# Kernel tuning notes

Measured on AMD Instinct MI355X. Metric: run time of the kernel, lower is better.

Reference implementation:

```python
import jax, jax.numpy as jnp
import numpy as np

N_NODES = 100000
N_EDGES = 640000
D_IN = 128
D_H = 128


def _lin_params(key, fan_in, fan_out):
    kw, kb = jax.random.split(key)
    s = 1.0 / np.sqrt(fan_in)
    W = jax.random.uniform(kw, (fan_in, fan_out), jnp.float32, -s, s)
    b = jax.random.uniform(kb, (fan_out,), jnp.float32, -s, s)
    return W, b


def setup_inputs() -> dict:
    key = jax.random.key(0)
    ks = jax.random.split(key, 9)
    x = jax.random.normal(ks[0], (N_NODES, D_IN), jnp.float32)
    edge_index = jax.random.randint(ks[1], (2, N_EDGES), 0, N_NODES, dtype=jnp.int64)
    W1, b1 = _lin_params(ks[2], D_IN, D_H)
    W2, b2 = _lin_params(ks[3], D_H, D_H)
    W3, b3 = _lin_params(ks[4], D_H, D_H)
    Wg0, bg0 = _lin_params(ks[5], D_H, D_H)
    Wg1, bg1 = _lin_params(ks[6], D_H, D_H)
    Wo, bo = _lin_params(ks[7], D_H, 1)
    return {"x": x, "edge_index": edge_index,
            "W1": W1, "b1": b1, "W2": W2, "b2": b2, "W3": W3, "b3": b3,
            "Wg0": Wg0, "bg0": bg0, "Wg1": Wg1, "bg1": bg1, "Wo": Wo, "bo": bo}


def gcn_conv(x, src, dst, W, b, n_nodes):
    """PyG GCNConv: D^{-1/2} (A+I) D^{-1/2} X W + b (self-loops added, sym norm)."""
    h = x @ W  # [N, F_out]
    # degree of A+I counted on target side (each self-loop adds 1)
    deg = jnp.zeros((n_nodes,), x.dtype).at[dst].add(1.0) + 1.0
    dis = jax.lax.rsqrt(deg)  # deg^{-1/2}
    coef = dis[src] * dis[dst]  # [E]
    agg = jax.ops.segment_sum(h[src] * coef[:, None], dst, num_segments=n_nodes)
    out = agg + h * (dis * dis)[:, None]  # self-loop term
    return out + b


def reference(x, edge_index, W1, b1, W2, b2, W3, b3, Wg0, bg0, Wg1, bg1, Wo, bo):
    src, dst = edge_index[0], edge_index[1]
    n = x.shape[0]
    lrelu = jax.nn.leaky_relu  # slope 0.01, matches torch default
    # feature extractor MLP
    h = lrelu(x @ W1 + b1)
    h = lrelu(h @ W2 + b2)
    h = lrelu(h @ W3 + b3)
    # input GCN
    h = lrelu(gcn_conv(h, src, dst, Wg0, bg0, n))
    # hidden GCN (dropout is identity in eval mode)
    h = lrelu(gcn_conv(h, src, dst, Wg1, bg1, n))
    # output GCN -> scalar per node
    return gcn_conv(h, src, dst, Wo, bo, n)
```

## Files before the change

kernel.cpp:

```cpp
#include <hip/hip_runtime.h>
#include <hip/hip_bf16.h>

#define D_H 128

typedef __attribute__((ext_vector_type(8))) short bf16x8;
typedef __attribute__((ext_vector_type(4))) float f32x4;

__device__ inline void trunc_split(float x, ushort& hi, ushort& lo) {
    uint u = __builtin_bit_cast(uint, x);
    hi = (ushort)(u >> 16);
    float fh = __builtin_bit_cast(float, u & 0xFFFF0000u);
    float fl = x - fh;
    lo = (ushort)(__builtin_bit_cast(uint, fl) >> 16);
}


__global__ __launch_bounds__(256)
void deg_count_int_kernel(const int* __restrict__ dst, int* __restrict__ cnt, int E) {
    int e = blockIdx.x * 256 + threadIdx.x;
    if (e < E) atomicAdd(&cnt[dst[e]], 1);
}

__global__ __launch_bounds__(256)
void dis_finalize_kernel(const int* __restrict__ cnt, float* __restrict__ dis, int M) {
    int i = blockIdx.x * 256 + threadIdx.x;
    if (i < M) dis[i] = rsqrtf((float)cnt[i] + 1.0f);
}

__global__ __launch_bounds__(256)
void scan_blocks_kernel(const int* __restrict__ cnt, int* __restrict__ rowptr,
                        int* __restrict__ aux, int M) {
    __shared__ int sdata[256];
    const int base = blockIdx.x * 1024 + threadIdx.x * 4;
    int v[4];
#pragma unroll
    for (int i = 0; i < 4; ++i) v[i] = (base + i < M) ? cnt[base + i] : 0;
    int tsum = v[0] + v[1] + v[2] + v[3];
    sdata[threadIdx.x] = tsum;
    __syncthreads();
    int val = tsum;
    for (int off = 1; off < 256; off <<= 1) {
        int n = (threadIdx.x >= off) ? sdata[threadIdx.x - off] : 0;
        __syncthreads();
        val += n;
        sdata[threadIdx.x] = val;
        __syncthreads();
    }
    int run = val - tsum;
#pragma unroll
    for (int i = 0; i < 4; ++i) {
        if (base + i < M) rowptr[base + i] = run;
        run += v[i];
    }
    if (threadIdx.x == 255) aux[blockIdx.x] = val;
}

__global__ __launch_bounds__(128)
void scan_aux_kernel(int* __restrict__ aux, int n) {
    __shared__ int s[128];
    int v = (threadIdx.x < n) ? aux[threadIdx.x] : 0;
    s[threadIdx.x] = v;
    __syncthreads();
    int val = v;
    for (int off = 1; off < 128; off <<= 1) {
        int nn = (threadIdx.x >= off) ? s[threadIdx.x - off] : 0;
        __syncthreads();
        val += nn;
        s[threadIdx.x] = val;
        __syncthreads();
    }
    if (threadIdx.x < n) aux[threadIdx.x] = val - v;
}

__global__ __launch_bounds__(256)
void scan_add_kernel(int* __restrict__ rowptr, int* __restrict__ cursor,
                     const int* __restrict__ aux, int M) {
    int i = blockIdx.x * 256 + threadIdx.x;
    if (i >= M) return;
    int v = rowptr[i] + aux[i >> 10];
    rowptr[i] = v;
    cursor[i] = v;
}

__global__ __launch_bounds__(256)
void scatter_kernel(const int* __restrict__ src, const int* __restrict__ dst,
                    const float* __restrict__ dis, int* __restrict__ cursor,
                    int* __restrict__ es, float* __restrict__ ces, int E) {
    int e = blockIdx.x * 256 + threadIdx.x;
    if (e >= E) return;
    int s = src[e], d = dst[e];
    int pos = atomicAdd(&cursor[d], 1);
    es[pos] = s;
    ces[pos] = dis[s];
}

__global__ __launch_bounds__(256)
void wprep_kernel(const float* __restrict__ W1, const float* __restrict__ W2,
                  const float* __restrict__ W3, const float* __restrict__ W4,
                  const float* __restrict__ W5, ushort* __restrict__ imgs) {
    int w = blockIdx.x >> 6;
    int e = (blockIdx.x & 63) * 256 + threadIdx.x;
    const float* W = w == 0 ? W1 : w == 1 ? W2 : w == 2 ? W3 : w == 3 ? W4 : W5;
    int k = e >> 7, n = e & 127;
    ushort hi, lo;
    trunc_split(W[e], hi, lo);
    ushort* img = imgs + (size_t)w * 34816;
    img[n * 136 + k]         = hi;
    img[17408 + n * 136 + k] = lo;
}

__global__ __launch_bounds__(512, 2)
void fused_mlp4_kernel(const float* __restrict__ X, const ushort* __restrict__ imgs,
                       const float* __restrict__ b1, const float* __restrict__ b2,
                       const float* __restrict__ b3, float* __restrict__ Y, int M) {
    __shared__ ushort sW[34816];
    __shared__ ushort sXhi[17408];
    __shared__ ushort sXlo[17408];

    const int tid  = threadIdx.x;
    const int lane = tid & 63;
    const int wv   = tid >> 6;
    const int bn   = lane & 15;
    const int g    = lane >> 4;
    const int kof  = g * 8;
    const int row0 = blockIdx.x * 128;
    const int lrow = wv * 16 + bn;
    const int arow = row0 + lrow;

    bf16x8 ahi[4], alo[4];
    {
        const bool ok = arow < M;
        const float* ap = X + (size_t)arow * 128 + kof;
#pragma unroll
        for (int kb = 0; kb < 4; ++kb) {
            float f[8];
            if (ok) {
                float4 f0 = *(const float4*)(ap + kb * 32);
                float4 f1 = *(const float4*)(ap + kb * 32 + 4);
                f[0] = f0.x; f[1] = f0.y; f[2] = f0.z; f[3] = f0.w;
                f[4] = f1.x; f[5] = f1.y; f[6] = f1.z; f[7] = f1.w;
            } else {
#pragma unroll
                for (int e = 0; e < 8; ++e) f[e] = 0.f;
            }
            bf16x8 h, l;
#pragma unroll
            for (int e = 0; e < 8; ++e) {
                ushort hb, lb;
                trunc_split(f[e], hb, lb);
                h[e] = (short)hb; l[e] = (short)lb;
            }
            ahi[kb] = h; alo[kb] = l;
        }
    }

    f32x4 acc[8];
    for (int t = 0; t < 4; ++t) {
        if (t > 0) __syncthreads();
        {
            const uint4* g4 = (const uint4*)(imgs + (size_t)t * 34816);
            uint4*       s4 = (uint4*)sW;
#pragma unroll
            for (int j = 0; j < 9; ++j) {
                int c = j * 512 + tid;
                if (c < 4352) s4[c] = g4[c];
            }
        }
        if (t > 0) {
#pragma unroll
            for (int kb = 0; kb < 4; ++kb) {
                ahi[kb] = *(const bf16x8*)&sXhi[lrow * 136 + kb * 32 + kof];
                alo[kb] = *(const bf16x8*)&sXlo[lrow * 136 + kb * 32 + kof];
            }
        }
        __syncthreads();

#pragma unroll
        for (int nt = 0; nt < 8; ++nt) acc[nt] = (f32x4){0.f, 0.f, 0.f, 0.f};
#pragma unroll
        for (int kb = 0; kb < 4; ++kb) {
#pragma unroll
            for (int nt = 0; nt < 8; ++nt) {
                const ushort* ph = &sW[(nt * 16 + bn) * 136 + kb * 32 + kof];
                bf16x8 bh = *(const bf16x8*)ph;
                bf16x8 bl = *(const bf16x8*)(ph + 17408);
                acc[nt] = __builtin_amdgcn_mfma_f32_16x16x32_bf16(ahi[kb], bh, acc[nt], 0, 0, 0);
                acc[nt] = __builtin_amdgcn_mfma_f32_16x16x32_bf16(alo[kb], bh, acc[nt], 0, 0, 0);
                acc[nt] = __builtin_amdgcn_mfma_f32_16x16x32_bf16(ahi[kb], bl, acc[nt], 0, 0, 0);
            }
        }

        if (t < 3) {
            const float* bias = t == 0 ? b1 : t == 1 ? b2 : b3;
#pragma unroll
            for (int nt = 0; nt < 8; ++nt) {
                int col = nt * 16 + bn;
                float bc = bias[col];
#pragma unroll
                for (int i = 0; i < 4; ++i) {
                    float v = acc[nt][i] + bc;
                    v = v > 0.f ? v : 0.01f * v;
                    ushort h, l;
                    trunc_split(v, h, l);
                    int r = wv * 16 + g * 4 + i;
                    sXhi[r * 136 + col] = h;
                    sXlo[r * 136 + col] = l;
                }
            }
        } else {
#pragma unroll
            for (int nt = 0; nt < 8; ++nt) {
                int col = nt * 16 + bn;
#pragma unroll
                for (int i = 0; i < 4; ++i) {
                    int row = row0 + wv * 16 + g * 4 + i;
                    if (row < M) Y[(size_t)row * 128 + col] = acc[nt][i];
                }
            }
        }
    }
}

__global__ __launch_bounds__(512, 4)
void gemm128_mfma_kernel(const float* __restrict__ X, const ushort* __restrict__ img,
                         float* __restrict__ Y, int M) {
    __shared__ ushort sB[34816];

    const int tid  = threadIdx.x;
    const int lane = tid & 63;
    const int wv   = tid >> 6;
    const int bn   = lane & 15;
    const int g    = lane >> 4;
    const int kof  = g * 8;
    const int row0 = blockIdx.x * 128;
    const int arow = row0 + wv * 16 + bn;

    {
        const uint4* g4 = (const uint4*)img;
        uint4*       s4 = (uint4*)sB;
#pragma unroll
        for (int j = 0; j < 9; ++j) {
            int c = j * 512 + tid;
            if (c < 4352) s4[c] = g4[c];
        }
    }

    bf16x8 ahi[4], alo[4];
    {
        const bool ok = arow < M;
        const float* ap = X + (size_t)arow * 128 + kof;
#pragma unroll
        for (int kb = 0; kb < 4; ++kb) {
            float f[8];
            if (ok) {
                float4 f0 = *(const float4*)(ap + kb * 32);
                float4 f1 = *(const float4*)(ap + kb * 32 + 4);
                f[0] = f0.x; f[1] = f0.y; f[2] = f0.z; f[3] = f0.w;
                f[4] = f1.x; f[5] = f1.y; f[6] = f1.z; f[7] = f1.w;
            } else {
#pragma unroll
                for (int e = 0; e < 8; ++e) f[e] = 0.f;
            }
            bf16x8 h, l;
#pragma unroll
            for (int e = 0; e < 8; ++e) {
                ushort hb, lb;
                trunc_split(f[e], hb, lb);
                h[e] = (short)hb; l[e] = (short)lb;
            }
            ahi[kb] = h; alo[kb] = l;
        }
    }
    __syncthreads();

    f32x4 acc[8];
#pragma unroll
    for (int nt = 0; nt < 8; ++nt) acc[nt] = (f32x4){0.f, 0.f, 0.f, 0.f};
#pragma unroll
    for (int kb = 0; kb < 4; ++kb) {
#pragma unroll
        for (int nt = 0; nt < 8; ++nt) {
            const ushort* ph = &sB[(nt * 16 + bn) * 136 + kb * 32 + kof];
            bf16x8 bh = *(const bf16x8*)ph;
            bf16x8 bl = *(const bf16x8*)(ph + 17408);
            acc[nt] = __builtin_amdgcn_mfma_f32_16x16x32_bf16(ahi[kb], bh, acc[nt], 0, 0, 0);
            acc[nt] = __builtin_amdgcn_mfma_f32_16x16x32_bf16(alo[kb], bh, acc[nt], 0, 0, 0);
            acc[nt] = __builtin_amdgcn_mfma_f32_16x16x32_bf16(ahi[kb], bl, acc[nt], 0, 0, 0);
        }
    }

#pragma unroll
    for (int nt = 0; nt < 8; ++nt) {
        int col = nt * 16 + bn;
#pragma unroll
        for (int i = 0; i < 4; ++i) {
            int row = row0 + wv * 16 + g * 4 + i;
            if (row < M) Y[(size_t)row * 128 + col] = acc[nt][i];
        }
    }
}

template<int MODE>
__global__ __launch_bounds__(256)
void gcn_agg_csr_kernel(const float* __restrict__ H, const int* __restrict__ es,
                        const float* __restrict__ ces, const int* __restrict__ rowptr,
                        const int* __restrict__ cnt, const float* __restrict__ dis,
                        const float* __restrict__ bias, const float* __restrict__ Wo,
                        float* __restrict__ Y, float* __restrict__ ho, int M) {
    int w    = (blockIdx.x * 256 + threadIdx.x) >> 6;
    int lane = threadIdx.x & 63;
    if (w >= M) return;

    const float dd  = dis[w];
    const int   beg = rowptr[w];
    const int   n   = cnt[w];

    float2 hv = ((const float2*)H)[(size_t)w * 64 + lane];
    float2 acc;
    acc.x = hv.x * dd * dd;
    acc.y = hv.y * dd * dd;

    int j = 0;
    for (; j + 4 <= n; j += 4) {
        int   s0 = es[beg + j],      s1 = es[beg + j + 1];
        int   s2 = es[beg + j + 2],  s3 = es[beg + j + 3];
        float c0 = ces[beg + j] * dd,     c1 = ces[beg + j + 1] * dd;
        float c2 = ces[beg + j + 2] * dd, c3 = ces[beg + j + 3] * dd;
        float2 v0 = ((const float2*)H)[(size_t)s0 * 64 + lane];
        float2 v1 = ((const float2*)H)[(size_t)s1 * 64 + lane];
        float2 v2 = ((const float2*)H)[(size_t)s2 * 64 + lane];
        float2 v3 = ((const float2*)H)[(size_t)s3 * 64 + lane];
        acc.x += c0 * v0.x + c1 * v1.x + c2 * v2.x + c3 * v3.x;
        acc.y += c0 * v0.y + c1 * v1.y + c2 * v2.y + c3 * v3.y;
    }
    for (; j < n; ++j) {
        int   s = es[beg + j];
        float c = ces[beg + j] * dd;
        float2 v = ((const float2*)H)[(size_t)s * 64 + lane];
        acc.x += c * v.x;
        acc.y += c * v.y;
    }

    float2 bb = ((const float2*)bias)[lane];
    acc.x += bb.x; acc.y += bb.y;
    acc.x = acc.x > 0.f ? acc.x : 0.01f * acc.x;
    acc.y = acc.y > 0.f ? acc.y : 0.01f * acc.y;

    if (MODE == 1) {
        ((float2*)Y)[(size_t)w * 64 + lane] = acc;
    } else {
        float2 wv = ((const float2*)Wo)[lane];
        float p = acc.x * wv.x + acc.y * wv.y;
#pragma unroll
        for (int off = 32; off > 0; off >>= 1) p += __shfl_down(p, off, 64);
        if (lane == 0) ho[w] = p;
    }
}

__global__ __launch_bounds__(256)
void out_csr_kernel(const float* __restrict__ ho, const int* __restrict__ es,
                    const float* __restrict__ ces, const int* __restrict__ rowptr,
                    const int* __restrict__ cnt, const float* __restrict__ dis,
                    const float* __restrict__ bo, float* __restrict__ out, int M) {
    int i = blockIdx.x * 256 + threadIdx.x;
    if (i >= M) return;
    float dd  = dis[i];
    float acc = ho[i] * dd * dd;
    int   beg = rowptr[i], n = cnt[i];
    for (int j = 0; j < n; ++j)
        acc += ces[beg + j] * dd * ho[es[beg + j]];
    out[i] = acc + bo[0];
}


extern "C" void kernel_launch(void* const* d_in, const int* in_sizes, int n_in,
                              void* d_out, int out_size, void* d_ws, size_t ws_size,
                              hipStream_t stream) {
    const float* x   = (const float*)d_in[0];
    const int*   ei  = (const int*)d_in[1];
    const float* W1  = (const float*)d_in[2];
    const float* b1  = (const float*)d_in[3];
    const float* W2  = (const float*)d_in[4];
    const float* b2  = (const float*)d_in[5];
    const float* W3  = (const float*)d_in[6];
    const float* b3  = (const float*)d_in[7];
    const float* Wg0 = (const float*)d_in[8];
    const float* bg0 = (const float*)d_in[9];
    const float* Wg1 = (const float*)d_in[10];
    const float* bg1 = (const float*)d_in[11];
    const float* Wo  = (const float*)d_in[12];
    const float* bo  = (const float*)d_in[13];

    const int M = in_sizes[0] / D_H;
    const int E = in_sizes[1] / 2;
    const int* se = ei;
    const int* de = ei + E;

    float*  A      = (float*)d_ws;
    float*  B      = A + (size_t)M * D_H;
    ushort* Wimg   = (ushort*)(B + (size_t)M * D_H);
    float*  dis    = (float*)(Wimg + 5 * 34816);
    float*  ho     = dis + M;
    float*  ces    = ho + M;
    int*    cnt    = (int*)(ces + E);
    int*    rowptr = cnt + M;
    int*    cursor = rowptr + M;
    int*    es     = cursor + M;
    int*    aux    = es + E;

    float* out = (float*)d_out;

    const int nChunks     = (M + 1023) / 1024;
    const int gemm_blocks = (M + 127) / 128;
    const int node_waves  = (M * 64 + 255) / 256;

    hipMemsetAsync(cnt, 0, M * sizeof(int), stream);
    wprep_kernel<<<320, 256, 0, stream>>>(W1, W2, W3, Wg0, Wg1, Wimg);
    deg_count_int_kernel<<<(E + 255) / 256, 256, 0, stream>>>(de, cnt, E);
    scan_blocks_kernel<<<nChunks, 256, 0, stream>>>(cnt, rowptr, aux, M);
    scan_aux_kernel<<<1, 128, 0, stream>>>(aux, nChunks);
    scan_add_kernel<<<(M + 255) / 256, 256, 0, stream>>>(rowptr, cursor, aux, M);
    dis_finalize_kernel<<<(M + 255) / 256, 256, 0, stream>>>(cnt, dis, M);
    scatter_kernel<<<(E + 255) / 256, 256, 0, stream>>>(se, de, dis, cursor, es, ces, E);

    fused_mlp4_kernel<<<gemm_blocks, 512, 0, stream>>>(x, Wimg, b1, b2, b3, B, M);

    gcn_agg_csr_kernel<1><<<node_waves, 256, 0, stream>>>(B, es, ces, rowptr, cnt, dis, bg0, nullptr, A, nullptr, M);

    gemm128_mfma_kernel<<<gemm_blocks, 512, 0, stream>>>(A, Wimg + 4 * 34816, B, M);

    gcn_agg_csr_kernel<2><<<node_waves, 256, 0, stream>>>(B, es, ces, rowptr, cnt, dis, bg1, Wo, nullptr, ho, M);

    out_csr_kernel<<<(M + 255) / 256, 256, 0, stream>>>(ho, es, ces, rowptr, cnt, dis, bo, out, M);
}
```

Before: 317.7 us.

## Cut fused MLP shared memory by aliasing activations and widen GEMM per-wave tiles

The fused MLP kernel drops its separate hi/lo activation buffers. It stages fp32 activations in the weight buffer, reloads them into registers and splits them to bf16 hi/lo there, with extra barriers. This cuts LDS use from about 139 KB to 70 KB so more blocks can fit per CU. The standalone GEMM now uses 256 threads, with each wave computing two 16-row groups that reuse every B fragment loaded from LDS. This halves LDS traffic per MFMA but raises register pressure.

```diff
diff --git a/kernel.cpp b/kernel.cpp
--- a/kernel.cpp
+++ b/kernel.cpp
@@ -109,13 +109,12 @@
     img[17408 + n * 136 + k] = lo;
 }
 
-__global__ __launch_bounds__(512, 2)
+__global__ __launch_bounds__(512, 4)
 void fused_mlp4_kernel(const float* __restrict__ X, const ushort* __restrict__ imgs,
                        const float* __restrict__ b1, const float* __restrict__ b2,
                        const float* __restrict__ b3, float* __restrict__ Y, int M) {
     __shared__ ushort sW[34816];
-    __shared__ ushort sXhi[17408];
-    __shared__ ushort sXlo[17408];
+    float* sAct = (float*)sW;
 
     const int tid  = threadIdx.x;
     const int lane = tid & 63;
@@ -125,10 +124,10 @@
     const int kof  = g * 8;
     const int row0 = blockIdx.x * 128;
     const int lrow = wv * 16 + bn;
-    const int arow = row0 + lrow;
 
     bf16x8 ahi[4], alo[4];
     {
+        const int arow = row0 + lrow;
         const bool ok = arow < M;
         const float* ap = X + (size_t)arow * 128 + kof;
 #pragma unroll
@@ -156,7 +155,6 @@
 
     f32x4 acc[8];
     for (int t = 0; t < 4; ++t) {
-        if (t > 0) __syncthreads();
         {
             const uint4* g4 = (const uint4*)(imgs + (size_t)t * 34816);
             uint4*       s4 = (uint4*)sW;
@@ -164,13 +162,6 @@
             for (int j = 0; j < 9; ++j) {
                 int c = j * 512 + tid;
                 if (c < 4352) s4[c] = g4[c];
-            }
-        }
-        if (t > 0) {
-#pragma unroll
-            for (int kb = 0; kb < 4; ++kb) {
-                ahi[kb] = *(const bf16x8*)&sXhi[lrow * 136 + kb * 32 + kof];
-                alo[kb] = *(const bf16x8*)&sXlo[lrow * 136 + kb * 32 + kof];
             }
         }
         __syncthreads();
@@ -191,6 +182,7 @@
         }
 
         if (t < 3) {
+            __syncthreads();
             const float* bias = t == 0 ? b1 : t == 1 ? b2 : b3;
 #pragma unroll
             for (int nt = 0; nt < 8; ++nt) {
@@ -200,13 +192,25 @@
                 for (int i = 0; i < 4; ++i) {
                     float v = acc[nt][i] + bc;
                     v = v > 0.f ? v : 0.01f * v;
-                    ushort h, l;
-                    trunc_split(v, h, l);
-                    int r = wv * 16 + g * 4 + i;
-                    sXhi[r * 136 + col] = h;
-                    sXlo[r * 136 + col] = l;
+                    sAct[(wv * 16 + g * 4 + i) * 132 + col] = v;
                 }
             }
+            __syncthreads();
+#pragma unroll
+            for (int kb = 0; kb < 4; ++kb) {
+                float4 f0 = *(const float4*)&sAct[lrow * 132 + kb * 32 + kof];
+                float4 f1 = *(const float4*)&sAct[lrow * 132 + kb * 32 + kof + 4];
+                float f[8] = {f0.x, f0.y, f0.z, f0.w, f1.x, f1.y, f1.z, f1.w};
+                bf16x8 h, l;
+#pragma unroll
+                for (int e = 0; e < 8; ++e) {
+                    ushort hb, lb;
+                    trunc_split(f[e], hb, lb);
+                    h[e] = (short)hb; l[e] = (short)lb;
+                }
+                ahi[kb] = h; alo[kb] = l;
+            }
+            __syncthreads();
         } else {
 #pragma unroll
             for (int nt = 0; nt < 8; ++nt) {
@@ -221,7 +225,7 @@
     }
 }
 
-__global__ __launch_bounds__(512, 4)
+__global__ __launch_bounds__(256, 2)
 void gemm128_mfma_kernel(const float* __restrict__ X, const ushort* __restrict__ img,
                          float* __restrict__ Y, int M) {
     __shared__ ushort sB[34816];
@@ -232,21 +236,19 @@
     const int bn   = lane & 15;
     const int g    = lane >> 4;
     const int kof  = g * 8;
-    const int row0 = blockIdx.x * 128;
-    const int arow = row0 + wv * 16 + bn;
+    const int row0 = blockIdx.x * 128 + wv * 32;
 
     {
         const uint4* g4 = (const uint4*)img;
         uint4*       s4 = (uint4*)sB;
 #pragma unroll
-        for (int j = 0; j < 9; ++j) {
-            int c = j * 512 + tid;
-            if (c < 4352) s4[c] = g4[c];
-        }
-    }
-
-    bf16x8 ahi[4], alo[4];
-    {
+        for (int j = 0; j < 17; ++j) s4[j * 256 + tid] = g4[j * 256 + tid];
+    }
+
+    bf16x8 ahi[2][4], alo[2][4];
+#pragma unroll
+    for (int rg = 0; rg < 2; ++rg) {
+        const int arow = row0 + rg * 16 + bn;
         const bool ok = arow < M;
         const float* ap = X + (size_t)arow * 128 + kof;
 #pragma unroll
@@ -268,14 +270,18 @@
                 trunc_split(f[e], hb, lb);
                 h[e] = (short)hb; l[e] = (short)lb;
             }
-            ahi[kb] = h; alo[kb] = l;
+            ahi[rg][kb] = h; alo[rg][kb] = l;
         }
     }
     __syncthreads();
 
-    f32x4 acc[8];
-#pragma unroll
-    for (int nt = 0; nt < 8; ++nt) acc[nt] = (f32x4){0.f, 0.f, 0.f, 0.f};
+    f32x4 acc0[8], acc1[8];
+#pragma unroll
+    for (int nt = 0; nt < 8; ++nt) {
+        acc0[nt] = (f32x4){0.f, 0.f, 0.f, 0.f};
+        acc1[nt] = (f32x4){0.f, 0.f, 0.f, 0.f};
+    }
+
 #pragma unroll
     for (int kb = 0; kb < 4; ++kb) {
 #pragma unroll
@@ -283,19 +289,27 @@
             const ushort* ph = &sB[(nt * 16 + bn) * 136 + kb * 32 + kof];
             bf16x8 bh = *(const bf16x8*)ph;
             bf16x8 bl = *(const bf16x8*)(ph + 17408);
-            acc[nt] = __builtin_amdgcn_mfma_f32_16x16x32_bf16(ahi[kb], bh, acc[nt], 0, 0, 0);
-            acc[nt] = __builtin_amdgcn_mfma_f32_16x16x32_bf16(alo[kb], bh, acc[nt], 0, 0, 0);
-            acc[nt] = __builtin_amdgcn_mfma_f32_16x16x32_bf16(ahi[kb], bl, acc[nt], 0, 0, 0);
-        }
-    }
-
-#pragma unroll
-    for (int nt = 0; nt < 8; ++nt) {
-        int col = nt * 16 + bn;
-#pragma unroll
-        for (int i = 0; i < 4; ++i) {
-            int row = row0 + wv * 16 + g * 4 + i;
-            if (row < M) Y[(size_t)row * 128 + col] = acc[nt][i];
+            acc0[nt] = __builtin_amdgcn_mfma_f32_16x16x32_bf16(ahi[0][kb], bh, acc0[nt], 0, 0, 0);
+            acc1[nt] = __builtin_amdgcn_mfma_f32_16x16x32_bf16(ahi[1][kb], bh, acc1[nt], 0, 0, 0);
+            acc0[nt] = __builtin_amdgcn_mfma_f32_16x16x32_bf16(alo[0][kb], bh, acc0[nt], 0, 0, 0);
+            acc1[nt] = __builtin_amdgcn_mfma_f32_16x16x32_bf16(alo[1][kb], bh, acc1[nt], 0, 0, 0);
+            acc0[nt] = __builtin_amdgcn_mfma_f32_16x16x32_bf16(ahi[0][kb], bl, acc0[nt], 0, 0, 0);
+            acc1[nt] = __builtin_amdgcn_mfma_f32_16x16x32_bf16(ahi[1][kb], bl, acc1[nt], 0, 0, 0);
+        }
+    }
+
+#pragma unroll
+    for (int rg = 0; rg < 2; ++rg) {
+        const f32x4* acc = rg == 0 ? acc0 : acc1;
+        const int rbase = row0 + rg * 16 + g * 4;
+#pragma unroll
+        for (int nt = 0; nt < 8; ++nt) {
+            int col = nt * 16 + bn;
+#pragma unroll
+            for (int i = 0; i < 4; ++i) {
+                int row = rbase + i;
+                if (row < M) Y[(size_t)row * 128 + col] = acc[nt][i];
+            }
         }
     }
 }
@@ -427,7 +441,7 @@
 
     gcn_agg_csr_kernel<1><<<node_waves, 256, 0, stream>>>(B, es, ces, rowptr, cnt, dis, bg0, nullptr, A, nullptr, M);
 
-    gemm128_mfma_kernel<<<gemm_blocks, 512, 0, stream>>>(A, Wimg + 4 * 34816, B, M);
+    gemm128_mfma_kernel<<<gemm_blocks, 256, 0, stream>>>(A, Wimg + 4 * 34816, B, M);
 
     gcn_agg_csr_kernel<2><<<node_waves, 256, 0, stream>>>(B, es, ces, rowptr, cnt, dis, bg1, Wo, nullptr, ho, M);
 
```

After: 294.5 us. 1.08x faster.

## Cut fused MLP LDS footprint, prefetch next weights in registers, fuse dis kernel

Applied to the files above, without the earlier changes.

The fused MLP kernel drops its separate hi/lo activation buffers and stages fp32 activations in the weight LDS buffer, so shared memory per block falls from about 140KB to 70KB. The launch bound is raised to allow more resident blocks. The next layer's weight image is prefetched into registers while the current layer's MFMAs run, and the plain GEMM kernel loads its weights the same way. The dis rsqrt computation is folded into scan_add, removing one launch. The costs are extra barriers and higher register pressure from the nine uint4 prefetch registers under the tighter launch bound.

```diff
diff --git a/kernel.cpp b/kernel.cpp
--- a/kernel.cpp
+++ b/kernel.cpp
@@ -19,12 +19,6 @@
 void deg_count_int_kernel(const int* __restrict__ dst, int* __restrict__ cnt, int E) {
     int e = blockIdx.x * 256 + threadIdx.x;
     if (e < E) atomicAdd(&cnt[dst[e]], 1);
-}
-
-__global__ __launch_bounds__(256)
-void dis_finalize_kernel(const int* __restrict__ cnt, float* __restrict__ dis, int M) {
-    int i = blockIdx.x * 256 + threadIdx.x;
-    if (i < M) dis[i] = rsqrtf((float)cnt[i] + 1.0f);
 }
 
 __global__ __launch_bounds__(256)
@@ -74,12 +68,14 @@
 
 __global__ __launch_bounds__(256)
 void scan_add_kernel(int* __restrict__ rowptr, int* __restrict__ cursor,
-                     const int* __restrict__ aux, int M) {
+                     const int* __restrict__ aux, const int* __restrict__ cnt,
+                     float* __restrict__ dis, int M) {
     int i = blockIdx.x * 256 + threadIdx.x;
     if (i >= M) return;
     int v = rowptr[i] + aux[i >> 10];
     rowptr[i] = v;
     cursor[i] = v;
+    dis[i] = rsqrtf((float)cnt[i] + 1.0f);
 }
 
 __global__ __launch_bounds__(256)
@@ -109,13 +105,12 @@
     img[17408 + n * 136 + k] = lo;
 }
 
-__global__ __launch_bounds__(512, 2)
+__global__ __launch_bounds__(512, 4)
 void fused_mlp4_kernel(const float* __restrict__ X, const ushort* __restrict__ imgs,
                        const float* __restrict__ b1, const float* __restrict__ b2,
                        const float* __restrict__ b3, float* __restrict__ Y, int M) {
     __shared__ ushort sW[34816];
-    __shared__ ushort sXhi[17408];
-    __shared__ ushort sXlo[17408];
+    float* sAct = (float*)sW;
 
     const int tid  = threadIdx.x;
     const int lane = tid & 63;
@@ -125,10 +120,20 @@
     const int kof  = g * 8;
     const int row0 = blockIdx.x * 128;
     const int lrow = wv * 16 + bn;
-    const int arow = row0 + lrow;
+
+    uint4 wreg[9];
+    {
+        const uint4* g4 = (const uint4*)imgs;
+#pragma unroll
+        for (int j = 0; j < 9; ++j) {
+            int c = j * 512 + tid;
+            wreg[j] = (c < 4352) ? g4[c] : make_uint4(0, 0, 0, 0);
+        }
+    }
 
     bf16x8 ahi[4], alo[4];
     {
+        const int arow = row0 + lrow;
         const bool ok = arow < M;
         const float* ap = X + (size_t)arow * 128 + kof;
 #pragma unroll
@@ -156,24 +161,24 @@
 
     f32x4 acc[8];
     for (int t = 0; t < 4; ++t) {
-        if (t > 0) __syncthreads();
         {
-            const uint4* g4 = (const uint4*)(imgs + (size_t)t * 34816);
-            uint4*       s4 = (uint4*)sW;
+            uint4* s4 = (uint4*)sW;
 #pragma unroll
             for (int j = 0; j < 9; ++j) {
                 int c = j * 512 + tid;
-                if (c < 4352) s4[c] = g4[c];
-            }
-        }
-        if (t > 0) {
-#pragma unroll
-            for (int kb = 0; kb < 4; ++kb) {
-                ahi[kb] = *(const bf16x8*)&sXhi[lrow * 136 + kb * 32 + kof];
-                alo[kb] = *(const bf16x8*)&sXlo[lrow * 136 + kb * 32 + kof];
+                if (c < 4352) s4[c] = wreg[j];
             }
         }
         __syncthreads();
+
+        if (t < 3) {
+            const uint4* g4 = (const uint4*)(imgs + (size_t)(t + 1) * 34816);
+#pragma unroll
+            for (int j = 0; j < 9; ++j) {
+                int c = j * 512 + tid;
+                wreg[j] = (c < 4352) ? g4[c] : make_uint4(0, 0, 0, 0);
+            }
+        }
 
 #pragma unroll
         for (int nt = 0; nt < 8; ++nt) acc[nt] = (f32x4){0.f, 0.f, 0.f, 0.f};
@@ -191,6 +196,7 @@
         }
 
         if (t < 3) {
+            __syncthreads();
             const float* bias = t == 0 ? b1 : t == 1 ? b2 : b3;
 #pragma unroll
             for (int nt = 0; nt < 8; ++nt) {
@@ -200,13 +206,24 @@
                 for (int i = 0; i < 4; ++i) {
                     float v = acc[nt][i] + bc;
                     v = v > 0.f ? v : 0.01f * v;
-                    ushort h, l;
-                    trunc_split(v, h, l);
-                    int r = wv * 16 + g * 4 + i;
-                    sXhi[r * 136 + col] = h;
-                    sXlo[r * 136 + col] = l;
+                    sAct[(wv * 16 + g * 4 + i) * 132 + col] = v;
                 }
             }
+#pragma unroll
+            for (int kb = 0; kb < 4; ++kb) {
+                float4 f0 = *(const float4*)&sAct[lrow * 132 + kb * 32 + kof];
+                float4 f1 = *(const float4*)&sAct[lrow * 132 + kb * 32 + kof + 4];
+                float f[8] = {f0.x, f0.y, f0.z, f0.w, f1.x, f1.y, f1.z, f1.w};
+                bf16x8 h, l;
+#pragma unroll
+                for (int e = 0; e < 8; ++e) {
+                    ushort hb, lb;
+                    trunc_split(f[e], hb, lb);
+                    h[e] = (short)hb; l[e] = (short)lb;
+                }
+                ahi[kb] = h; alo[kb] = l;
+            }
+            __syncthreads();
         } else {
 #pragma unroll
             for (int nt = 0; nt < 8; ++nt) {
@@ -235,13 +252,13 @@
     const int row0 = blockIdx.x * 128;
     const int arow = row0 + wv * 16 + bn;
 
+    uint4 wreg[9];
     {
         const uint4* g4 = (const uint4*)img;
-        uint4*       s4 = (uint4*)sB;
 #pragma unroll
         for (int j = 0; j < 9; ++j) {
             int c = j * 512 + tid;
-            if (c < 4352) s4[c] = g4[c];
+            wreg[j] = (c < 4352) ? g4[c] : make_uint4(0, 0, 0, 0);
         }
     }
 
@@ -269,6 +286,15 @@
                 h[e] = (short)hb; l[e] = (short)lb;
             }
             ahi[kb] = h; alo[kb] = l;
+        }
+    }
+
+    {
+        uint4* s4 = (uint4*)sB;
+#pragma unroll
+        for (int j = 0; j < 9; ++j) {
+            int c = j * 512 + tid;
+            if (c < 4352) s4[c] = wreg[j];
         }
     }
     __syncthreads();
@@ -419,8 +445,7 @@
     deg_count_int_kernel<<<(E + 255) / 256, 256, 0, stream>>>(de, cnt, E);
     scan_blocks_kernel<<<nChunks, 256, 0, stream>>>(cnt, rowptr, aux, M);
     scan_aux_kernel<<<1, 128, 0, stream>>>(aux, nChunks);
-    scan_add_kernel<<<(M + 255) / 256, 256, 0, stream>>>(rowptr, cursor, aux, M);
-    dis_finalize_kernel<<<(M + 255) / 256, 256, 0, stream>>>(cnt, dis, M);
+    scan_add_kernel<<<(M + 255) / 256, 256, 0, stream>>>(rowptr, cursor, aux, cnt, dis, M);
     scatter_kernel<<<(E + 255) / 256, 256, 0, stream>>>(se, de, dis, cursor, es, ces, E);
 
     fused_mlp4_kernel<<<gemm_blocks, 512, 0, stream>>>(x, Wimg, b1, b2, b3, B, M);
```

Result: slower. 345.0 us (+8.6%).
